# Optimization experiments

Measured on AMD Instinct MI355X. Metric: run time of the kernel, lower is better.

Reference implementation:

```python
import jax, jax.numpy as jnp
import numpy as np

B, T, OMNI_D, STATIC_D = 128, 1024, 32, 16
H = 64            # hidden // 2 (per-direction GRU size)
HID = 128         # hidden
PHYS_LEN, N_PHYS = 432, 5


def _gelu(x):
    return jax.nn.gelu(x, approximate=False)  # torch GELU default = exact erf


def _ln(x, g, b, eps=1e-5):
    m = jnp.mean(x, -1, keepdims=True)
    v = jnp.var(x, -1, keepdims=True)
    return (x - m) / jnp.sqrt(v + eps) * g + b


def _gru_layer(x, Wih, Whh, bih, bhh, reverse):
    # PyTorch GRU cell math; x: [B,T,D] -> (outputs [B,T,H], h_final [B,H])
    Hh = Whh.shape[1]
    gi = jnp.einsum('btd,gd->btg', x, Wih) + bih  # precompute input projections
    if reverse:
        gi = gi[:, ::-1]
    gi = jnp.swapaxes(gi, 0, 1)  # [T,B,3H]
    h0 = jnp.zeros((x.shape[0], Hh), x.dtype)

    def step(h, g):
        gh = h @ Whh.T + bhh
        r = jax.nn.sigmoid(g[:, :Hh] + gh[:, :Hh])
        z = jax.nn.sigmoid(g[:, Hh:2 * Hh] + gh[:, Hh:2 * Hh])
        n = jnp.tanh(g[:, 2 * Hh:] + r * gh[:, 2 * Hh:])
        hn = (1 - z) * n + z * h
        return hn, hn

    hT, ys = jax.lax.scan(step, h0, gi)
    ys = jnp.swapaxes(ys, 0, 1)
    if reverse:
        ys = ys[:, ::-1]
    return ys, hT


def _conv1d(x, W, b, pad, dil):
    y = jax.lax.conv_general_dilated(x, W, (1,), [(pad, pad)], rhs_dilation=(dil,),
                                     dimension_numbers=('NCH', 'OIH', 'NCH'))
    return y + b[None, :, None]


def setup_inputs():
    key = jax.random.key(0)
    ks = iter(jax.random.split(key, 64))

    def rn(shape, s=0.05):
        return jax.random.normal(next(ks), shape, jnp.float32) * s

    inp = {
        'omni_seq': rn((B, T, OMNI_D), 1.0),
        'static_x': rn((B, STATIC_D), 1.0),
        'phys': rn((B, N_PHYS, PHYS_LEN), 1.0),
    }
    for l, d_in in (('l0', OMNI_D), ('l1', 2 * H)):
        for dr in ('f', 'b'):
            inp[f'gru_Wih_{l}{dr}'] = rn((3 * H, d_in))
            inp[f'gru_Whh_{l}{dr}'] = rn((3 * H, H))
            inp[f'gru_bih_{l}{dr}'] = rn((3 * H,))
            inp[f'gru_bhh_{l}{dr}'] = rn((3 * H,))
    inp['sm_W'] = rn((H, STATIC_D)); inp['sm_b'] = rn((H,))
    inp['sm_ln_g'] = jnp.ones((H,), jnp.float32); inp['sm_ln_b'] = jnp.zeros((H,), jnp.float32)
    inp['gate_W'] = rn((N_PHYS, H)); inp['gate_b'] = rn((N_PHYS,))
    inp['attn_in_W'] = rn((3 * N_PHYS, N_PHYS)); inp['attn_in_b'] = rn((3 * N_PHYS,))
    inp['attn_out_W'] = rn((N_PHYS, N_PHYS)); inp['attn_out_b'] = rn((N_PHYS,))
    for i, ksz in ((1, 3), (2, 5), (3, 9)):
        inp[f'conv{i}_W'] = rn((HID // 4, N_PHYS, ksz)); inp[f'conv{i}_b'] = rn((HID // 4,))
    FUSED = HID + H + 3 * (HID // 4)  # 288
    inp['head_ln_g'] = jnp.ones((FUSED,), jnp.float32); inp['head_ln_b'] = jnp.zeros((FUSED,), jnp.float32)
    inp['head_W1'] = rn((HID, FUSED)); inp['head_b1'] = rn((HID,))
    inp['head_W2'] = rn((PHYS_LEN, HID)); inp['head_b2'] = rn((PHYS_LEN,))
    return inp


def reference(omni_seq, static_x, phys,
              gru_Wih_l0f, gru_Whh_l0f, gru_bih_l0f, gru_bhh_l0f,
              gru_Wih_l0b, gru_Whh_l0b, gru_bih_l0b, gru_bhh_l0b,
              gru_Wih_l1f, gru_Whh_l1f, gru_bih_l1f, gru_bhh_l1f,
              gru_Wih_l1b, gru_Whh_l1b, gru_bih_l1b, gru_bhh_l1b,
              sm_W, sm_b, sm_ln_g, sm_ln_b, gate_W, gate_b,
              attn_in_W, attn_in_b, attn_out_W, attn_out_b,
              conv1_W, conv1_b, conv2_W, conv2_b, conv3_W, conv3_b,
              head_ln_g, head_ln_b, head_W1, head_b1, head_W2, head_b2):
    # --- bidirectional 2-layer GRU (eval mode: dropout off) ---
    y0f, _ = _gru_layer(omni_seq, gru_Wih_l0f, gru_Whh_l0f, gru_bih_l0f, gru_bhh_l0f, False)
    y0b, _ = _gru_layer(omni_seq, gru_Wih_l0b, gru_Whh_l0b, gru_bih_l0b, gru_bhh_l0b, True)
    x1 = jnp.concatenate([y0f, y0b], -1)
    _, hf = _gru_layer(x1, gru_Wih_l1f, gru_Whh_l1f, gru_bih_l1f, gru_bhh_l1f, False)
    _, hb = _gru_layer(x1, gru_Wih_l1b, gru_Whh_l1b, gru_bih_l1b, gru_bhh_l1b, True)
    omni_embed = jnp.concatenate([hf, hb], -1)  # h_omni[-2] ++ h_omni[-1], [B,128]
    # --- static MLP ---
    static_embed = _ln(_gelu(static_x @ sm_W.T + sm_b), sm_ln_g, sm_ln_b)  # [B,64]
    # --- gating on phys channels ---
    gates = jax.nn.sigmoid(static_embed @ gate_W.T + gate_b)[..., None]  # [B,5,1]
    p = phys * gates  # [B,5,432]
    # --- tiny MHA: embed_dim=5, 5 heads, head_dim=1 -> scale = 1/sqrt(1) = 1 ---
    pt = jnp.swapaxes(p, 1, 2)  # [B,432,5]
    qkv = pt @ attn_in_W.T + attn_in_b
    E = N_PHYS
    q, k, v = qkv[..., :E], qkv[..., E:2 * E], qkv[..., 2 * E:]
    scores = jnp.einsum('bih,bjh->bhij', q, k)  # [B,5,432,432]
    attn = jax.nn.softmax(scores, -1)
    ao = jnp.einsum('bhij,bjh->bih', attn, v)
    ao = ao @ attn_out_W.T + attn_out_b  # out_proj
    p = jnp.swapaxes(ao, 1, 2)  # [B,5,432]
    # --- dilated conv branches + GELU + adaptive avg pool (= mean over length) ---
    c1 = _gelu(_conv1d(p, conv1_W, conv1_b, 1, 1)).mean(-1)
    c2 = _gelu(_conv1d(p, conv2_W, conv2_b, 2, 2)).mean(-1)
    c3 = _gelu(_conv1d(p, conv3_W, conv3_b, 4, 4)).mean(-1)
    fused = jnp.concatenate([omni_embed, static_embed, c1, c2, c3], 1)  # [B,288]
    h = _ln(fused, head_ln_g, head_ln_b)
    h = _gelu(h @ head_W1.T + head_b1)  # dropout off in eval
    return h @ head_W2.T + head_b2  # [B,432]
```

## Files before the change

### kernel.cpp

```cpp
#include <hip/hip_runtime.h>
#include <stdint.h>

#define B_ 128
#define T_ 1024
#define BT_ (B_*T_)
#define H_ 64
#define G_ 192
#define PL_ 432
#define NP_ 5
#define FUSED_ 288
#define N_IN 41

typedef unsigned short u16;
typedef __attribute__((ext_vector_type(8))) short bf16x8;
typedef __attribute__((ext_vector_type(4))) float f32x4;
typedef _Float16 h2 __attribute__((ext_vector_type(2)));
typedef _Float16 h8 __attribute__((ext_vector_type(8)));

__device__ inline float bf2f(u16 u){ union{float f; unsigned int i;} c; c.i = ((unsigned int)u)<<16; return c.f; }
__device__ inline u16 f2bf(float f){ unsigned int u = __float_as_uint(f); unsigned int r = (u + 0x7fffu + ((u>>16)&1u))>>16; return (u16)r; }
__device__ inline _Float16 bf2h(u16 u){ return (_Float16)bf2f(u); }
__device__ inline float sigm(float x){ return 1.f/(1.f+__expf(-x)); }
__device__ inline float tanh_(float x){ float t = __expf(fminf(fmaxf(2.f*x,-30.f),30.f)); return (t-1.f)/(t+1.f); }
__device__ inline float gelu_(float x){ return 0.5f*x*(1.f + erff(x*0.70710678118654752f)); }
__device__ inline float wredsum(float v){
  #pragma unroll
  for(int o=32;o>0;o>>=1) v += __shfl_xor(v,o);
  return v;
}

#if __has_builtin(__builtin_amdgcn_fdot2)
__device__ inline float dot2(h2 a, h2 b, float c){ return __builtin_amdgcn_fdot2(a, b, c, false); }
#else
__device__ inline float dot2(h2 a, h2 b, float c){ return c + (float)a.x*(float)b.x + (float)a.y*(float)b.y; }
#endif

struct CvtArgs {
  const void* src[N_IN];
  unsigned dstOff[N_IN];
  unsigned cnt[N_IN];
  unsigned blkStart[N_IN+1];
};

__global__ __launch_bounds__(256) void convert_k(CvtArgs a, u16* __restrict__ dst){
  const bool isbf = (((const u16*)a.src[21])[0] == 0x3F80u);
  int b = blockIdx.x;
  int lo = 0, hi = N_IN;
  while (hi - lo > 1){ int mid = (lo+hi)>>1; if (a.blkStart[mid] <= (unsigned)b) lo = mid; else hi = mid; }
  const int i = lo;
  const unsigned lb = (unsigned)b - a.blkStart[i];
  const unsigned n = a.cnt[i];
  u16* d = dst + a.dstOff[i];
  if (isbf){
    const u16* s = (const u16*)a.src[i];
    #pragma unroll
    for(int e=0;e<8;e++){ unsigned idx = lb*2048u + e*256u + threadIdx.x; if (idx < n) d[idx] = s[idx]; }
  } else {
    const float* s = (const float*)a.src[i];
    #pragma unroll
    for(int e=0;e<8;e++){ unsigned idx = lb*2048u + e*256u + threadIdx.x; if (idx < n) d[idx] = f2bf(s[idx]); }
  }
}

template<int K>
__global__ __launch_bounds__(256) void gi_gemm(const u16* __restrict__ A,
    const u16* __restrict__ Wf, const u16* __restrict__ Wb,
    const u16* __restrict__ biasF, const u16* __restrict__ biasB,
    u16* __restrict__ out)
{
  const int wv = threadIdx.x >> 6, lane = threadIdx.x & 63;
  const int l15 = lane & 15, quad = lane >> 4;
  const size_t mBase = (size_t)blockIdx.x*64 + wv*16;

  bf16x8 afr[K/32];
  #pragma unroll
  for(int kc=0;kc<K/32;kc++)
    afr[kc] = *(const bf16x8*)(A + (mBase + l15)*K + kc*32 + quad*8);

  #pragma unroll
  for(int half=0; half<2; ++half){
    const u16* W    = half ? Wb : Wf;
    const u16* bias = half ? biasB : biasF;
    u16* o = out + (size_t)half * BT_ * G_;
    for(int nt=0; nt<12; ++nt){
      int n = nt*16 + l15;
      f32x4 acc = {0.f,0.f,0.f,0.f};
      #pragma unroll
      for(int kc=0;kc<K/32;kc++){
        bf16x8 bfr = *(const bf16x8*)(W + n*K + kc*32 + quad*8);
        acc = __builtin_amdgcn_mfma_f32_16x16x32_bf16(afr[kc], bfr, acc, 0,0,0);
      }
      float bv = bf2f(bias[n]);
      #pragma unroll
      for(int r=0;r<4;r++){
        size_t row = mBase + quad*4 + r;
        o[row*G_ + n] = f2bf(acc[r] + bv);
      }
    }
  }
}

__global__ __launch_bounds__(64)
__attribute__((amdgpu_waves_per_eu(1,1)))
void recur(const u16* __restrict__ gi,
    const u16* __restrict__ WhF, const u16* __restrict__ WhB,
    const u16* __restrict__ bhF, const u16* __restrict__ bhB,
    u16* __restrict__ y_x1, float* __restrict__ hfin, int layer)
{
  const int chain = blockIdx.x;
  const int dir = chain >> 7;
  const int b = chain & 127;
  const int j = threadIdx.x;
  const u16* Wh = dir ? WhB : WhF;
  const u16* bh = dir ? bhB : bhF;

  h2 wr[32], wz[32], wn[32];
  #pragma unroll
  for(int k8=0;k8<8;k8++){
    uint4 q;
    q = *(const uint4*)(Wh + (size_t)j*64 + k8*8);
    wr[4*k8+0] = (h2){bf2h((u16)(q.x&0xffffu)), bf2h((u16)(q.x>>16))};
    wr[4*k8+1] = (h2){bf2h((u16)(q.y&0xffffu)), bf2h((u16)(q.y>>16))};
    wr[4*k8+2] = (h2){bf2h((u16)(q.z&0xffffu)), bf2h((u16)(q.z>>16))};
    wr[4*k8+3] = (h2){bf2h((u16)(q.w&0xffffu)), bf2h((u16)(q.w>>16))};
    q = *(const uint4*)(Wh + (size_t)(64+j)*64 + k8*8);
    wz[4*k8+0] = (h2){bf2h((u16)(q.x&0xffffu)), bf2h((u16)(q.x>>16))};
    wz[4*k8+1] = (h2){bf2h((u16)(q.y&0xffffu)), bf2h((u16)(q.y>>16))};
    wz[4*k8+2] = (h2){bf2h((u16)(q.z&0xffffu)), bf2h((u16)(q.z>>16))};
    wz[4*k8+3] = (h2){bf2h((u16)(q.w&0xffffu)), bf2h((u16)(q.w>>16))};
    q = *(const uint4*)(Wh + (size_t)(128+j)*64 + k8*8);
    wn[4*k8+0] = (h2){bf2h((u16)(q.x&0xffffu)), bf2h((u16)(q.x>>16))};
    wn[4*k8+1] = (h2){bf2h((u16)(q.y&0xffffu)), bf2h((u16)(q.y>>16))};
    wn[4*k8+2] = (h2){bf2h((u16)(q.z&0xffffu)), bf2h((u16)(q.z>>16))};
    wn[4*k8+3] = (h2){bf2h((u16)(q.w&0xffffu)), bf2h((u16)(q.w>>16))};
  }
  const float bhr = bf2f(bh[j]), bhz = bf2f(bh[64+j]), bhn = bf2f(bh[128+j]);

  __shared__ __align__(16) u16 giLds[2][3072];
  __shared__ _Float16 hSf[64];
  h8* hS8 = (h8*)hSf;
  hSf[j] = (_Float16)0.f;

  const u16* giC = gi + (size_t)chain * T_ * G_;

  auto issue_chunk = [&](int c, int buf){
    int tbase = dir ? (1008 - c*16) : (c*16);
    const u16* src = giC + (size_t)tbase*G_ + j*8;
    u16* dst = &giLds[buf][0];
    #pragma unroll
    for(int i=0;i<6;i++){
      __builtin_amdgcn_global_load_lds(
        (const __attribute__((address_space(1))) void*)(src + i*512),
        (__attribute__((address_space(3))) void*)(dst + i*512), 16, 0, 0);
    }
  };

  issue_chunk(0, 0);

  float h = 0.f;
  for(int c=0; c<64; ++c){
    asm volatile("s_waitcnt vmcnt(0)" ::: "memory");
    if (c < 63) issue_chunk(c+1, (c+1)&1);
    const u16* gbuf = &giLds[c&1][0];
    #pragma unroll 2
    for(int ls=0; ls<16; ++ls){
      int row = dir ? (15-ls) : ls;
      const u16* rowp = gbuf + row*G_;
      float r0=bhr, r1=0.f, z0=bhz, z1=0.f, n0=bhn, n1=0.f;
      #pragma unroll
      for(int k=0;k<8;k++){
        h8 hv = hS8[k];
        h2 p0 = __builtin_shufflevector(hv, hv, 0, 1);
        h2 p1 = __builtin_shufflevector(hv, hv, 2, 3);
        h2 p2 = __builtin_shufflevector(hv, hv, 4, 5);
        h2 p3 = __builtin_shufflevector(hv, hv, 6, 7);
        r0 = dot2(wr[4*k+0], p0, r0); r1 = dot2(wr[4*k+1], p1, r1);
        r0 = dot2(wr[4*k+2], p2, r0); r1 = dot2(wr[4*k+3], p3, r1);
        z0 = dot2(wz[4*k+0], p0, z0); z1 = dot2(wz[4*k+1], p1, z1);
        z0 = dot2(wz[4*k+2], p2, z0); z1 = dot2(wz[4*k+3], p3, z1);
        n0 = dot2(wn[4*k+0], p0, n0); n1 = dot2(wn[4*k+1], p1, n1);
        n0 = dot2(wn[4*k+2], p2, n0); n1 = dot2(wn[4*k+3], p3, n1);
      }
      float gr = bf2f(rowp[j]), gz = bf2f(rowp[64+j]), gn = bf2f(rowp[128+j]);

      float r  = sigm(gr + (r0+r1));
      float z  = sigm(gz + (z0+z1));
      float nn = tanh_(gn + r*(n0+n1));
      h = (1.f - z)*nn + z*h;

      hSf[j] = (_Float16)h;

      if (layer == 0){
        int s = c*16 + ls;
        int t = dir ? (T_-1-s) : s;
        y_x1[((size_t)b*T_ + t)*128 + dir*64 + j] = f2bf(h);
      }
    }
  }
  if (layer == 1) hfin[b*FUSED_ + dir*64 + j] = h;
}

__global__ __launch_bounds__(448) void staticqkv_k(const u16* __restrict__ sx,
   const u16* __restrict__ smW, const u16* __restrict__ smb,
   const u16* __restrict__ lng, const u16* __restrict__ lnb,
   const u16* __restrict__ gW, const u16* __restrict__ gb,
   const u16* __restrict__ phys, const u16* __restrict__ aW,
   const u16* __restrict__ ab,
   float* __restrict__ fused, float* __restrict__ qkv)
{
  int b = blockIdx.x, tid = threadIdx.x;
  __shared__ float gS[5];
  if (tid < 64){
    int j = tid;
    float xr[16];
    #pragma unroll
    for(int k=0;k<16;k++) xr[k] = bf2f(sx[b*16+k]);
    float acc = bf2f(smb[j]);
    #pragma unroll
    for(int k=0;k<16;k++) acc += xr[k]*bf2f(smW[j*16+k]);
    float xg = gelu_(acc);
    float m = wredsum(xg)*(1.f/64.f);
    float d = xg - m;
    float v = wredsum(d*d)*(1.f/64.f);
    float se = d*rsqrtf(v+1e-5f)*bf2f(lng[j]) + bf2f(lnb[j]);
    fused[b*FUSED_ + 128 + j] = se;
    #pragma unroll
    for(int i=0;i<5;i++){
      float p = se*bf2f(gW[i*64+j]);
      float s = wredsum(p);
      if (j == 0) gS[i] = sigm(s + bf2f(gb[i]));
    }
  }
  __syncthreads();
  int l = tid;
  if (l < PL_){
    float pv[5];
    #pragma unroll
    for(int i=0;i<5;i++) pv[i] = bf2f(phys[((size_t)b*5+i)*PL_ + l]) * gS[i];
    #pragma unroll
    for(int c=0;c<15;c++){
      float a = bf2f(ab[c]);
      #pragma unroll
      for(int i=0;i<5;i++) a += pv[i]*bf2f(aW[c*5+i]);
      qkv[((size_t)b*15+c)*PL_ + l] = a;
    }
  }
}

__global__ __launch_bounds__(256) void attn_k(const float* __restrict__ qkv,
                                              float* __restrict__ ao)
{
  int h = blockIdx.x, b = blockIdx.y;
  int tid = threadIdx.x;
  __shared__ float kS[PL_], vS[PL_];
  __shared__ float red[32];
  const float* qb = qkv + ((size_t)b*15 + h)*PL_;
  const float* kb = qkv + ((size_t)b*15 + 5 + h)*PL_;
  const float* vb = qkv + ((size_t)b*15 + 10 + h)*PL_;
  for(int j=tid;j<PL_;j+=256){ kS[j]=kb[j]; vS[j]=vb[j]; }
  __syncthreads();
  float lmax=-1e30f, lmin=1e30f;
  for(int j=tid;j<PL_;j+=256){ float kv=kS[j]; lmax=fmaxf(lmax,kv); lmin=fminf(lmin,kv); }
  #pragma unroll
  for(int o=32;o>0;o>>=1){ lmax=fmaxf(lmax,__shfl_xor(lmax,o)); lmin=fminf(lmin,__shfl_xor(lmin,o)); }
  int wv = tid>>6;
  if ((tid&63)==0){ red[wv]=lmax; red[8+wv]=lmin; }
  __syncthreads();
  if (tid==0){
    float mx=red[0], mn=red[8];
    for(int i=1;i<4;i++){ mx=fmaxf(mx,red[i]); mn=fminf(mn,red[8+i]); }
    red[16]=mx; red[17]=mn;
  }
  __syncthreads();
  float kmx=red[16], kmn=red[17];
  for(int i=tid;i<PL_;i+=256){
    float s = qb[i];
    float m = fmaxf(s*kmx, s*kmn);
    float den=0.f, num=0.f;
    #pragma unroll 4
    for(int j=0;j<PL_;j++){
      float e = __expf(s*kS[j]-m);
      den += e; num += e*vS[j];
    }
    ao[((size_t)b*PL_+i)*5 + h] = num/den;
  }
}

template<int KS, int DIL, int PAD>
__device__ inline void do_conv(const float* pS, const u16* Wc, const u16* bc,
                               float* fused, int b, int o, int p, int cslot)
{
  const int Lout = PL_ + 2*PAD - DIL*(KS-1);
  float w[5][KS];
  #pragma unroll
  for(int i=0;i<5;i++)
    #pragma unroll
    for(int t=0;t<KS;t++) w[i][t] = bf2f(Wc[(o*5+i)*KS + t]);
  float bias = bf2f(bc[o]);
  float acc = 0.f;
  for(int l=p; l<Lout; l+=8){
    float s = bias;
    #pragma unroll
    for(int t=0;t<KS;t++){
      int idx = l - PAD + t*DIL;
      if (idx >= 0 && idx < PL_){
        #pragma unroll
        for(int i=0;i<5;i++) s += w[i][t]*pS[i*PL_ + idx];
      }
    }
    acc += gelu_(s);
  }
  #pragma unroll
  for(int off=1;off<8;off<<=1) acc += __shfl_xor(acc,off);
  if (p == 0) fused[b*FUSED_ + 192 + cslot*32 + o] = acc/(float)Lout;
}

__global__ __launch_bounds__(256) void projconv_k(const float* __restrict__ ao,
  const u16* __restrict__ oW, const u16* __restrict__ ob,
  const u16* __restrict__ W1c, const u16* __restrict__ b1c,
  const u16* __restrict__ W2c, const u16* __restrict__ b2c,
  const u16* __restrict__ W3c, const u16* __restrict__ b3c,
  float* __restrict__ fused)
{
  int b = blockIdx.x, tid = threadIdx.x;
  __shared__ float pS[5*PL_];
  for(int l=tid; l<PL_; l+=256){
    float a[5];
    #pragma unroll
    for(int hh=0;hh<5;hh++) a[hh] = ao[((size_t)b*PL_+l)*5 + hh];
    #pragma unroll
    for(int c=0;c<5;c++){
      float s = bf2f(ob[c]);
      #pragma unroll
      for(int hh=0;hh<5;hh++) s += a[hh]*bf2f(oW[c*5+hh]);
      pS[c*PL_ + l] = s;
    }
  }
  __syncthreads();
  int o = tid >> 3, p = tid & 7;
  do_conv<3,1,1>(pS, W1c, b1c, fused, b, o, p, 0);
  do_conv<5,2,2>(pS, W2c, b2c, fused, b, o, p, 1);
  do_conv<9,4,4>(pS, W3c, b3c, fused, b, o, p, 2);
}

__global__ __launch_bounds__(448) void head_k(const float* __restrict__ fused,
   const u16* __restrict__ lng, const u16* __restrict__ lnb,
   const u16* __restrict__ W1, const u16* __restrict__ b1,
   const u16* __restrict__ W2, const u16* __restrict__ b2,
   void* __restrict__ out, const u16* __restrict__ detect)
{
  const bool isbf = (detect[0] == 0x3F80u);
  int b = blockIdx.x, tid = threadIdx.x;
  __shared__ float fS[FUSED_];
  __shared__ float hS[128];
  __shared__ float red[32];
  float v = (tid < FUSED_) ? fused[b*FUSED_ + tid] : 0.f;
  float s1 = wredsum(v);
  float s2 = wredsum(v*v);
  int wv = tid>>6;
  if ((tid&63)==0){ red[wv]=s1; red[8+wv]=s2; }
  __syncthreads();
  if (tid==0){
    float S=0.f, SS=0.f;
    for(int i=0;i<7;i++){ S+=red[i]; SS+=red[8+i]; }
    float m = S/288.f;
    red[16]=m; red[17]=SS/288.f - m*m;
  }
  __syncthreads();
  float m = red[16], var = red[17];
  if (tid < FUSED_) fS[tid] = (v-m)*rsqrtf(var+1e-5f)*bf2f(lng[tid]) + bf2f(lnb[tid]);
  __syncthreads();
  if (tid < 128){
    float a = bf2f(b1[tid]);
    const u16* wr = W1 + (size_t)tid*FUSED_;
    #pragma unroll
    for(int k8=0;k8<36;k8++){
      uint4 q = *(const uint4*)(wr + k8*8);
      a += fS[8*k8+0]*bf2f((u16)(q.x&0xffffu)) + fS[8*k8+1]*bf2f((u16)(q.x>>16))
         + fS[8*k8+2]*bf2f((u16)(q.y&0xffffu)) + fS[8*k8+3]*bf2f((u16)(q.y>>16))
         + fS[8*k8+4]*bf2f((u16)(q.z&0xffffu)) + fS[8*k8+5]*bf2f((u16)(q.z>>16))
         + fS[8*k8+6]*bf2f((u16)(q.w&0xffffu)) + fS[8*k8+7]*bf2f((u16)(q.w>>16));
    }
    hS[tid] = gelu_(a);
  }
  __syncthreads();
  if (tid < PL_){
    float a = bf2f(b2[tid]);
    const u16* wr = W2 + (size_t)tid*128;
    #pragma unroll
    for(int k8=0;k8<16;k8++){
      uint4 q = *(const uint4*)(wr + k8*8);
      a += hS[8*k8+0]*bf2f((u16)(q.x&0xffffu)) + hS[8*k8+1]*bf2f((u16)(q.x>>16))
         + hS[8*k8+2]*bf2f((u16)(q.y&0xffffu)) + hS[8*k8+3]*bf2f((u16)(q.y>>16))
         + hS[8*k8+4]*bf2f((u16)(q.z&0xffffu)) + hS[8*k8+5]*bf2f((u16)(q.z>>16))
         + hS[8*k8+6]*bf2f((u16)(q.w&0xffffu)) + hS[8*k8+7]*bf2f((u16)(q.w>>16));
    }
    size_t oi = (size_t)b*PL_ + tid;
    if (isbf) ((u16*)out)[oi] = f2bf(a);
    else      ((float*)out)[oi] = a;
  }
}

extern "C" void kernel_launch(void* const* d_in, const int* in_sizes, int n_in,
                              void* d_out, int out_size, void* d_ws, size_t ws_size,
                              hipStream_t stream)
{
  static const unsigned cnts[N_IN] = {
    4194304, 2048, 276480,
    6144, 12288, 192, 192,
    6144, 12288, 192, 192,
    24576, 12288, 192, 192,
    24576, 12288, 192, 192,
    1024, 64, 64, 64,
    320, 5,
    75, 15,
    25, 5,
    480, 32, 800, 32, 1440, 32,
    288, 288,
    36864, 128, 55296, 432
  };

  char* ws = (char*)d_ws;
  size_t off = 0;
  auto alloc = [&](size_t bytes){ size_t o = off; off = (off + bytes + 255) & ~(size_t)255; return o; };

  CvtArgs ca;
  const u16* cin[N_IN];
  unsigned totalBlocks = 0;
  for (int i=0;i<N_IN;i++){
    ca.src[i] = d_in[i];
    ca.cnt[i] = cnts[i];
    size_t o = alloc((size_t)cnts[i]*2);
    ca.dstOff[i] = (unsigned)(o/2);
    cin[i] = (const u16*)(ws + o);
    ca.blkStart[i] = totalBlocks;
    totalBlocks += (cnts[i] + 2047u)/2048u;
  }
  ca.blkStart[N_IN] = totalBlocks;
  u16* canon = (u16*)ws;

  u16*   gi    = (u16*)  (ws + alloc((size_t)2*BT_*G_*2));
  u16*   x1    = (u16*)  (ws + alloc((size_t)BT_*128*2));
  float* fused = (float*)(ws + alloc((size_t)B_*FUSED_*4));
  float* qkv   = (float*)(ws + alloc((size_t)B_*15*PL_*4));
  float* ao    = (float*)(ws + alloc((size_t)B_*PL_*5*4));
  (void)ws_size; (void)in_sizes; (void)n_in; (void)out_size;

  convert_k<<<totalBlocks, 256, 0, stream>>>(ca, canon);

  gi_gemm<32><<<BT_/64, 256, 0, stream>>>(cin[0], cin[3], cin[7], cin[5], cin[9], gi);
  recur<<<256, 64, 0, stream>>>(gi, cin[4], cin[8], cin[6], cin[10], x1, nullptr, 0);
  gi_gemm<128><<<BT_/64, 256, 0, stream>>>(x1, cin[11], cin[15], cin[13], cin[17], gi);
  recur<<<256, 64, 0, stream>>>(gi, cin[12], cin[16], cin[14], cin[18], nullptr, fused, 1);
  staticqkv_k<<<128, 448, 0, stream>>>(cin[1], cin[19], cin[20], cin[21], cin[22],
                                       cin[23], cin[24], cin[2], cin[25], cin[26],
                                       fused, qkv);
  attn_k<<<dim3(5,128), 256, 0, stream>>>(qkv, ao);
  projconv_k<<<128, 256, 0, stream>>>(ao, cin[27], cin[28], cin[29], cin[30],
                                      cin[31], cin[32], cin[33], cin[34], fused);
  head_k<<<128, 448, 0, stream>>>(fused, cin[35], cin[36], cin[37], cin[38], cin[39], cin[40],
                                  d_out, (const u16*)d_in[21]);
}
```

Before: 1.256 ms.

## Process two batch chains per GRU recurrence block to interleave dependency chains

Each single-wave recurrence block now advances two independent batch sequences of the same direction together, sharing the register-resident recurrent weights and double-buffered LDS staging of input projections. The grid shrinks from 256 to 128 blocks. The aim is to hide the per-step serial latency (LDS round trip, dot products, transcendentals) by interleaving two independent chains. The cost is half as many CUs in use and doubled per-step instruction work per wave, plus higher register pressure.

Result: slower. 1.921 ms (+52.9%).

```diff
diff --git a/kernel.cpp b/kernel.cpp
--- a/kernel.cpp
+++ b/kernel.cpp
@@ -107,9 +107,12 @@
     const u16* __restrict__ bhF, const u16* __restrict__ bhB,
     u16* __restrict__ y_x1, float* __restrict__ hfin, int layer)
 {
-  const int chain = blockIdx.x;
-  const int dir = chain >> 7;
-  const int b = chain & 127;
+  const int blk = blockIdx.x;
+  const int dir = blk >> 6;
+  const int bA = blk & 63;
+  const int bB = bA + 64;
+  const int chainA = dir*128 + bA;
+  const int chainB = dir*128 + bB;
   const int j = threadIdx.x;
   const u16* Wh = dir ? WhB : WhF;
   const u16* bh = dir ? bhB : bhF;
@@ -136,68 +139,101 @@
   }
   const float bhr = bf2f(bh[j]), bhz = bf2f(bh[64+j]), bhn = bf2f(bh[128+j]);
 
-  __shared__ __align__(16) u16 giLds[2][3072];
-  __shared__ _Float16 hSf[64];
-  h8* hS8 = (h8*)hSf;
-  hSf[j] = (_Float16)0.f;
-
-  const u16* giC = gi + (size_t)chain * T_ * G_;
+  __shared__ __align__(16) u16 giLds[2][2][3072];
+  __shared__ __align__(16) _Float16 hSfA[64];
+  __shared__ __align__(16) _Float16 hSfB[64];
+  h8* hS8A = (h8*)hSfA;
+  h8* hS8B = (h8*)hSfB;
+  hSfA[j] = (_Float16)0.f;
+  hSfB[j] = (_Float16)0.f;
+
+  const u16* giA = gi + (size_t)chainA * T_ * G_;
+  const u16* giB = gi + (size_t)chainB * T_ * G_;
 
   auto issue_chunk = [&](int c, int buf){
     int tbase = dir ? (1008 - c*16) : (c*16);
-    const u16* src = giC + (size_t)tbase*G_ + j*8;
-    u16* dst = &giLds[buf][0];
+    const u16* sA = giA + (size_t)tbase*G_ + j*8;
+    const u16* sB = giB + (size_t)tbase*G_ + j*8;
+    u16* dA = &giLds[0][buf][0];
+    u16* dB = &giLds[1][buf][0];
     #pragma unroll
     for(int i=0;i<6;i++){
       __builtin_amdgcn_global_load_lds(
-        (const __attribute__((address_space(1))) void*)(src + i*512),
-        (__attribute__((address_space(3))) void*)(dst + i*512), 16, 0, 0);
+        (const __attribute__((address_space(1))) void*)(sA + i*512),
+        (__attribute__((address_space(3))) void*)(dA + i*512), 16, 0, 0);
+      __builtin_amdgcn_global_load_lds(
+        (const __attribute__((address_space(1))) void*)(sB + i*512),
+        (__attribute__((address_space(3))) void*)(dB + i*512), 16, 0, 0);
     }
   };
 
   issue_chunk(0, 0);
 
-  float h = 0.f;
+  float hA = 0.f, hB = 0.f;
   for(int c=0; c<64; ++c){
     asm volatile("s_waitcnt vmcnt(0)" ::: "memory");
     if (c < 63) issue_chunk(c+1, (c+1)&1);
-    const u16* gbuf = &giLds[c&1][0];
+    const u16* gbA = &giLds[0][c&1][0];
+    const u16* gbB = &giLds[1][c&1][0];
     #pragma unroll 2
     for(int ls=0; ls<16; ++ls){
       int row = dir ? (15-ls) : ls;
-      const u16* rowp = gbuf + row*G_;
-      float r0=bhr, r1=0.f, z0=bhz, z1=0.f, n0=bhn, n1=0.f;
+      const u16* rpA = gbA + row*G_;
+      const u16* rpB = gbB + row*G_;
+      float r0A=bhr, r1A=0.f, z0A=bhz, z1A=0.f, n0A=bhn, n1A=0.f;
+      float r0B=bhr, r1B=0.f, z0B=bhz, z1B=0.f, n0B=bhn, n1B=0.f;
       #pragma unroll
       for(int k=0;k<8;k++){
-        h8 hv = hS8[k];
-        h2 p0 = __builtin_shufflevector(hv, hv, 0, 1);
-        h2 p1 = __builtin_shufflevector(hv, hv, 2, 3);
-        h2 p2 = __builtin_shufflevector(hv, hv, 4, 5);
-        h2 p3 = __builtin_shufflevector(hv, hv, 6, 7);
-        r0 = dot2(wr[4*k+0], p0, r0); r1 = dot2(wr[4*k+1], p1, r1);
-        r0 = dot2(wr[4*k+2], p2, r0); r1 = dot2(wr[4*k+3], p3, r1);
-        z0 = dot2(wz[4*k+0], p0, z0); z1 = dot2(wz[4*k+1], p1, z1);
-        z0 = dot2(wz[4*k+2], p2, z0); z1 = dot2(wz[4*k+3], p3, z1);
-        n0 = dot2(wn[4*k+0], p0, n0); n1 = dot2(wn[4*k+1], p1, n1);
-        n0 = dot2(wn[4*k+2], p2, n0); n1 = dot2(wn[4*k+3], p3, n1);
+        h8 hvA = hS8A[k];
+        h8 hvB = hS8B[k];
+        h2 a0 = __builtin_shufflevector(hvA, hvA, 0, 1);
+        h2 a1 = __builtin_shufflevector(hvA, hvA, 2, 3);
+        h2 a2 = __builtin_shufflevector(hvA, hvA, 4, 5);
+        h2 a3 = __builtin_shufflevector(hvA, hvA, 6, 7);
+        h2 b0 = __builtin_shufflevector(hvB, hvB, 0, 1);
+        h2 b1 = __builtin_shufflevector(hvB, hvB, 2, 3);
+        h2 b2 = __builtin_shufflevector(hvB, hvB, 4, 5);
+        h2 b3 = __builtin_shufflevector(hvB, hvB, 6, 7);
+        r0A = dot2(wr[4*k+0], a0, r0A); r0B = dot2(wr[4*k+0], b0, r0B);
+        r1A = dot2(wr[4*k+1], a1, r1A); r1B = dot2(wr[4*k+1], b1, r1B);
+        r0A = dot2(wr[4*k+2], a2, r0A); r0B = dot2(wr[4*k+2], b2, r0B);
+        r1A = dot2(wr[4*k+3], a3, r1A); r1B = dot2(wr[4*k+3], b3, r1B);
+        z0A = dot2(wz[4*k+0], a0, z0A); z0B = dot2(wz[4*k+0], b0, z0B);
+        z1A = dot2(wz[4*k+1], a1, z1A); z1B = dot2(wz[4*k+1], b1, z1B);
+        z0A = dot2(wz[4*k+2], a2, z0A); z0B = dot2(wz[4*k+2], b2, z0B);
+        z1A = dot2(wz[4*k+3], a3, z1A); z1B = dot2(wz[4*k+3], b3, z1B);
+        n0A = dot2(wn[4*k+0], a0, n0A); n0B = dot2(wn[4*k+0], b0, n0B);
+        n1A = dot2(wn[4*k+1], a1, n1A); n1B = dot2(wn[4*k+1], b1, n1B);
+        n0A = dot2(wn[4*k+2], a2, n0A); n0B = dot2(wn[4*k+2], b2, n0B);
+        n1A = dot2(wn[4*k+3], a3, n1A); n1B = dot2(wn[4*k+3], b3, n1B);
       }
-      float gr = bf2f(rowp[j]), gz = bf2f(rowp[64+j]), gn = bf2f(rowp[128+j]);
-
-      float r  = sigm(gr + (r0+r1));
-      float z  = sigm(gz + (z0+z1));
-      float nn = tanh_(gn + r*(n0+n1));
-      h = (1.f - z)*nn + z*h;
-
-      hSf[j] = (_Float16)h;
+      float grA = bf2f(rpA[j]), gzA = bf2f(rpA[64+j]), gnA = bf2f(rpA[128+j]);
+      float grB = bf2f(rpB[j]), gzB = bf2f(rpB[64+j]), gnB = bf2f(rpB[128+j]);
+
+      float rA  = sigm(grA + (r0A+r1A));
+      float rB  = sigm(grB + (r0B+r1B));
+      float zA  = sigm(gzA + (z0A+z1A));
+      float zB  = sigm(gzB + (z0B+z1B));
+      float nnA = tanh_(gnA + rA*(n0A+n1A));
+      float nnB = tanh_(gnB + rB*(n0B+n1B));
+      hA = (1.f - zA)*nnA + zA*hA;
+      hB = (1.f - zB)*nnB + zB*hB;
+
+      hSfA[j] = (_Float16)hA;
+      hSfB[j] = (_Float16)hB;
 
       if (layer == 0){
         int s = c*16 + ls;
         int t = dir ? (T_-1-s) : s;
-        y_x1[((size_t)b*T_ + t)*128 + dir*64 + j] = f2bf(h);
+        y_x1[((size_t)bA*T_ + t)*128 + dir*64 + j] = f2bf(hA);
+        y_x1[((size_t)bB*T_ + t)*128 + dir*64 + j] = f2bf(hB);
       }
     }
   }
-  if (layer == 1) hfin[b*FUSED_ + dir*64 + j] = h;
+  if (layer == 1){
+    hfin[bA*FUSED_ + dir*64 + j] = hA;
+    hfin[bB*FUSED_ + dir*64 + j] = hB;
+  }
 }
 
 __global__ __launch_bounds__(448) void staticqkv_k(const u16* __restrict__ sx,
@@ -449,9 +485,9 @@
   convert_k<<<totalBlocks, 256, 0, stream>>>(ca, canon);
 
   gi_gemm<32><<<BT_/64, 256, 0, stream>>>(cin[0], cin[3], cin[7], cin[5], cin[9], gi);
-  recur<<<256, 64, 0, stream>>>(gi, cin[4], cin[8], cin[6], cin[10], x1, nullptr, 0);
+  recur<<<128, 64, 0, stream>>>(gi, cin[4], cin[8], cin[6], cin[10], x1, nullptr, 0);
   gi_gemm<128><<<BT_/64, 256, 0, stream>>>(x1, cin[11], cin[15], cin[13], cin[17], gi);
-  recur<<<256, 64, 0, stream>>>(gi, cin[12], cin[16], cin[14], cin[18], nullptr, fused, 1);
+  recur<<<128, 64, 0, stream>>>(gi, cin[12], cin[16], cin[14], cin[18], nullptr, fused, 1);
   staticqkv_k<<<128, 448, 0, stream>>>(cin[1], cin[19], cin[20], cin[21], cin[22],
                                        cin[23], cin[24], cin[2], cin[25], cin[26],
                                        fused, qkv);
```
